# Kernel optimization log

Hardware: AMD Instinct MI355X
Metric: run time of the kernel (lower is better)

The kernel has to match this reference:

```python
import jax, jax.numpy as jnp
import numpy as np

EMBED_DIM = 768
NUM_HEADS = 12
HEAD_DIM = EMBED_DIM // NUM_HEADS
B, S = 2, 2048


def setup_inputs() -> dict:
    key = jax.random.key(0)
    k1, k2, k3, k4, k5 = jax.random.split(key, 5)
    scale = 1.0 / np.sqrt(EMBED_DIM)
    return {
        "x": jax.random.normal(k1, (B, S, EMBED_DIM), dtype=jnp.float32),
        "w_qkv": jax.random.normal(k2, (EMBED_DIM, 3 * EMBED_DIM), dtype=jnp.float32) * scale,
        "b_qkv": jax.random.normal(k3, (3 * EMBED_DIM,), dtype=jnp.float32) * 0.01,
        "w_proj": jax.random.normal(k4, (EMBED_DIM, EMBED_DIM), dtype=jnp.float32) * scale,
        "b_proj": jax.random.normal(k5, (EMBED_DIM,), dtype=jnp.float32) * 0.01,
    }


def reference(x, w_qkv, b_qkv, w_proj, b_proj):
    b, s, e = x.shape
    h, d = NUM_HEADS, HEAD_DIM
    # fused QKV projection: [b, s, 3, h, d]
    qkv = (x @ w_qkv + b_qkv).reshape(b, s, 3, h, d)
    q = qkv[:, :, 0].transpose(0, 2, 1, 3)  # [b, h, s, d]
    k = qkv[:, :, 1].transpose(0, 2, 1, 3)
    v = qkv[:, :, 2].transpose(0, 2, 1, 3)
    scores = jnp.einsum("bhqd,bhkd->bhqk", q, k) * (d ** -0.5)
    attn = jax.nn.softmax(scores, axis=-1)  # dropout is identity in eval mode
    out = jnp.einsum("bhqk,bhkd->bhqd", attn, v)
    out = out.transpose(0, 2, 1, 3).reshape(b, s, e)
    return out @ w_proj + b_proj
```

## Files before the change

### kernel.cpp

```cpp
#include <hip/hip_runtime.h>
#include <hip/hip_bf16.h>


typedef __bf16 bf16x8 __attribute__((ext_vector_type(8)));
typedef float f32x4 __attribute__((ext_vector_type(4)));
typedef unsigned short ushortx8 __attribute__((ext_vector_type(8)));
typedef unsigned short ushortx4 __attribute__((ext_vector_type(4)));
typedef unsigned int uintx4 __attribute__((ext_vector_type(4)));

#define EMB 768
#define SEQ 2048
#define NHEAD 12
#define HDIM 64
#define MROWS 4096
#define NQKV 2304
#define QSCALE 0.18033688011112042f

static __device__ __forceinline__ unsigned short b16(float f) {
  __hip_bfloat16 h = __float2bfloat16(f);
  return __builtin_bit_cast(unsigned short, h);
}

static __device__ __forceinline__ unsigned int cvtpk(float lo, float hi) {
  unsigned int r;
  asm("v_cvt_pk_bf16_f32 %0, %1, %2" : "=v"(r) : "v"(lo), "v"(hi));
  return r;
}

static __device__ __forceinline__ void gld16(const void* g, void* l) {
  __builtin_amdgcn_global_load_lds((const __attribute__((address_space(1))) void*)g,
                                   (__attribute__((address_space(3))) void*)l, 16, 0, 0);
}

__global__ __launch_bounds__(256) void k_prep(
    const float* __restrict__ x, const float* __restrict__ wqkv, const float* __restrict__ wproj,
    unsigned short* __restrict__ xb, unsigned short* __restrict__ wqkvT,
    unsigned short* __restrict__ wprojT) {
  __shared__ float t[64][65];
  const int bid = blockIdx.x;
  const int tid = threadIdx.x;
  if (bid < 1536) {
    int i = (bid * 256 + tid) * 8;
    f32x4 v0 = *(const f32x4*)(x + i);
    f32x4 v1 = *(const f32x4*)(x + i + 4);
    ushortx8 o;
    o[0] = b16(v0[0]); o[1] = b16(v0[1]); o[2] = b16(v0[2]); o[3] = b16(v0[3]);
    o[4] = b16(v1[0]); o[5] = b16(v1[1]); o[6] = b16(v1[2]); o[7] = b16(v1[3]);
    *(ushortx8*)(xb + i) = o;
    return;
  }
  const float* in; unsigned short* out; int N, bx, by;
  if (bid < 1536 + 432) { in = wqkv;  out = wqkvT;  N = NQKV; int r = bid - 1536; bx = r % 36; by = r / 36; }
  else                  { in = wproj; out = wprojT; N = EMB;  int r = bid - 1968; bx = r % 12; by = r / 12; }
  const int n0 = bx * 64, k0 = by * 64;
  const int xx = tid & 63, y0 = tid >> 6;
  #pragma unroll
  for (int i = 0; i < 16; ++i) { int r = y0 * 16 + i; t[r][xx] = in[(size_t)(k0 + r) * N + n0 + xx]; }
  __syncthreads();
  const int ks = tid & 7;
  const int nr0 = tid >> 3;
  #pragma unroll
  for (int i = 0; i < 2; ++i) {
    int nr = nr0 + i * 32;
    ushortx8 o;
    #pragma unroll
    for (int j = 0; j < 8; ++j) o[j] = b16(t[ks * 8 + j][nr]);
    *(ushortx8*)(out + (size_t)(n0 + nr) * EMB + k0 + ks * 8) = o;
  }
}

static __device__ __forceinline__ void gemm_tile_128(
    const unsigned short* __restrict__ A, const unsigned short* __restrict__ B,
    int K, int bm, int bn, char* lA, char* lB, f32x4 acc[4][4]) {
  const int tid = threadIdx.x, lane = tid & 63, w = tid >> 6;
  const int l15 = lane & 15, lg = lane >> 4;
  const int wm = w >> 1, wn = w & 1;
  #pragma unroll
  for (int m = 0; m < 4; ++m)
    #pragma unroll
    for (int n = 0; n < 4; ++n)
      acc[m][n] = (f32x4){0.f, 0.f, 0.f, 0.f};

  const int srow = w * 32 + (lane >> 3);
  const int glog = (lane & 7) ^ (lane >> 3);
  const size_t abase = (size_t)(bm * 128 + srow) * K + glog * 8;
  const size_t bbase = (size_t)(bn * 128 + srow) * K + glog * 8;
  const char* aB = lA + (wm * 64 + l15) * 128;
  const char* bB = lB + (wn * 64 + l15) * 128;
  const int rsw = (l15 & 7) << 4;

  const int T = K >> 6;
  {
    char* ad = lA + w * 4096; char* bd = lB + w * 4096;
    #pragma unroll
    for (int j = 0; j < 4; ++j) {
      gld16(A + abase + (size_t)j * 8 * K, ad + j * 1024);
      gld16(B + bbase + (size_t)j * 8 * K, bd + j * 1024);
    }
  }
  for (int t = 0; t < T; ++t) {
    const int cur = t & 1;
    if (t + 1 < T) {
      const int k1 = (t + 1) << 6;
      char* ad = lA + (cur ^ 1) * 16384 + w * 4096;
      char* bd = lB + (cur ^ 1) * 16384 + w * 4096;
      #pragma unroll
      for (int j = 0; j < 4; ++j) {
        gld16(A + abase + (size_t)j * 8 * K + k1, ad + j * 1024);
        gld16(B + bbase + (size_t)j * 8 * K + k1, bd + j * 1024);
      }
      asm volatile("s_waitcnt vmcnt(8)" ::: "memory");
    } else {
      asm volatile("s_waitcnt vmcnt(0)" ::: "memory");
    }
    __builtin_amdgcn_s_barrier();
    const char* ab = aB + cur * 16384;
    const char* bb = bB + cur * 16384;
    bf16x8 af[2][4], bfr[2][4];
    #pragma unroll
    for (int kk = 0; kk < 2; ++kk) {
      #pragma unroll
      for (int m = 0; m < 4; ++m)
        af[kk][m] = *(const bf16x8*)(ab + m * 2048 + (((kk * 4 + lg) * 16) ^ rsw));
      #pragma unroll
      for (int n = 0; n < 4; ++n)
        bfr[kk][n] = *(const bf16x8*)(bb + n * 2048 + (((kk * 4 + lg) * 16) ^ rsw));
    }
    #pragma unroll
    for (int kk = 0; kk < 2; ++kk)
      #pragma unroll
      for (int m = 0; m < 4; ++m)
        #pragma unroll
        for (int n = 0; n < 4; ++n)
          acc[m][n] = __builtin_amdgcn_mfma_f32_16x16x32_bf16(af[kk][m], bfr[kk][n], acc[m][n], 0, 0, 0);
    if (t + 1 < T) __builtin_amdgcn_s_barrier();
  }
}

static __device__ __forceinline__ int kvperm(int s) {
  return (s & ~0x1C) | ((s & 0x0C) << 1) | ((s & 0x10) >> 2);
}

__global__ __launch_bounds__(256) void k_gemm_qkv(
    const unsigned short* __restrict__ Xb, const unsigned short* __restrict__ Wt,
    const float* __restrict__ bias,
    unsigned short* __restrict__ Qb, unsigned short* __restrict__ Kb,
    unsigned short* __restrict__ VTb) {
  __shared__ __align__(16) char Alds[2 * 16384];
  __shared__ __align__(16) char Blds[2 * 16384];
  f32x4 acc[4][4];
  const int bm = blockIdx.x, bn = blockIdx.y;
  gemm_tile_128(Xb, Wt, EMB, bm, bn, Alds, Blds, acc);
  const int tid = threadIdx.x, lane = tid & 63, w = tid >> 6;
  const int l15 = lane & 15, lg = lane >> 4, wm = w >> 1, wn = w & 1;
  const int treg = bn / 6;
  if (treg < 2) {
    #pragma unroll
    for (int m = 0; m < 4; ++m)
      #pragma unroll
      for (int n = 0; n < 4; ++n)
        #pragma unroll
        for (int r = 0; r < 4; ++r) {
          int gr = bm * 128 + wm * 64 + m * 16 + lg * 4 + r;
          int gc = bn * 128 + wn * 64 + n * 16 + l15;
          float v = acc[m][n][r] + bias[gc];
          int rem = gc - treg * 768;
          int h = rem >> 6, d = rem & 63;
          int b = gr >> 11, s = gr & 2047;
          size_t off = ((size_t)(b * 12 + h) * 2048 + s) * 64 + d;
          if (treg == 0) Qb[off] = b16(v * QSCALE);
          else           Kb[off] = b16(v);
        }
  } else {
    #pragma unroll
    for (int m = 0; m < 4; ++m)
      #pragma unroll
      for (int n = 0; n < 4; ++n) {
        int gr0 = bm * 128 + wm * 64 + m * 16 + lg * 4;
        int gc = bn * 128 + wn * 64 + n * 16 + l15;
        int rem = gc - 1536;
        int h = rem >> 6, d = rem & 63;
        int b = gr0 >> 11, s0 = gr0 & 2047;
        int sp0 = kvperm(s0);
        ushortx4 o;
        #pragma unroll
        for (int r = 0; r < 4; ++r) o[r] = b16(acc[m][n][r] + bias[gc]);
        *(ushortx4*)(VTb + ((size_t)(b * 12 + h) * 64 + d) * 2048 + sp0) = o;
      }
  }
}

__global__ __launch_bounds__(256) void k_gemm_proj(
    const unsigned short* __restrict__ Ab, const unsigned short* __restrict__ Wt,
    const float* __restrict__ bias, float* __restrict__ out) {
  __shared__ __align__(16) char Alds[2 * 16384];
  __shared__ __align__(16) char Blds[2 * 16384];
  f32x4 acc[4][4];
  const int bm = blockIdx.x, bn = blockIdx.y;
  gemm_tile_128(Ab, Wt, EMB, bm, bn, Alds, Blds, acc);
  const int tid = threadIdx.x, lane = tid & 63, w = tid >> 6;
  const int l15 = lane & 15, lg = lane >> 4, wm = w >> 1, wn = w & 1;
  #pragma unroll
  for (int m = 0; m < 4; ++m)
    #pragma unroll
    for (int n = 0; n < 4; ++n)
      #pragma unroll
      for (int r = 0; r < 4; ++r) {
        int gr = bm * 128 + wm * 64 + m * 16 + lg * 4 + r;
        int gc = bn * 128 + wn * 64 + n * 16 + l15;
        out[(size_t)gr * EMB + gc] = acc[m][n][r] + bias[gc];
      }
}

__global__ __launch_bounds__(256) void k_attn(
    const unsigned short* __restrict__ Qg, const unsigned short* __restrict__ Kg,
    const unsigned short* __restrict__ VTg, unsigned short* __restrict__ AO) {
  __shared__ __align__(16) char KL[3 * 8192];
  __shared__ __align__(16) char VTL[3 * 8192];
  const int bid = blockIdx.x;
  const int slot = bid >> 3;
  const int bh = (bid & 7) * 3 + slot / 32;
  const int qt = slot & 31;
  const int b = bh / 12, h = bh % 12;
  const size_t base = (size_t)bh * (SEQ * HDIM);
  const int tid = threadIdx.x, lane = tid & 63, w = tid >> 6;
  const int l15 = lane & 15, lg = lane >> 4;
  const int swz = (l15 & 7) << 4;

  bf16x8 qf[2];
  {
    const size_t qoff = base + (size_t)(qt * 64 + w * 16 + l15) * 64 + lg * 8;
    qf[0] = *(const bf16x8*)(Qg + qoff);
    qf[1] = *(const bf16x8*)(Qg + qoff + 32);
  }

  const int srow0 = tid >> 3;
  const int scg0 = (tid & 7) ^ (srow0 & 7);
  const int scg1 = (tid & 7) ^ ((srow0 + 32) & 7);

  #define ASTAGE(tt, buf) do {                                                         \
    const int kv_ = (tt) * 64;                                                         \
    char* kd_ = KL + (buf) * 8192 + w * 1024;                                          \
    char* vd_ = VTL + (buf) * 8192 + w * 1024;                                         \
    gld16(Kg + base + (size_t)(kv_ + srow0) * 64 + scg0 * 8,           kd_);           \
    gld16(Kg + base + (size_t)(kv_ + srow0 + 32) * 64 + scg1 * 8,      kd_ + 4096);    \
    gld16(VTg + base + (size_t)srow0 * 2048 + kv_ + scg0 * 8,          vd_);           \
    gld16(VTg + base + (size_t)(srow0 + 32) * 2048 + kv_ + scg1 * 8,   vd_ + 4096);    \
  } while (0)

  f32x4 Oacc[4];
  #pragma unroll
  for (int nd = 0; nd < 4; ++nd) Oacc[nd] = (f32x4){0.f, 0.f, 0.f, 0.f};
  float l_ = 0.f;

  ASTAGE(0, 0);
  ASTAGE(1, 1);
  asm volatile("s_waitcnt vmcnt(4)" ::: "memory");
  __builtin_amdgcn_s_barrier();

  int cur = 0, pre = 2;
  for (int t = 0; t < 32; ++t) {
    if (t + 2 < 32) ASTAGE(t + 2, pre);
    const char* kb = KL + cur * 8192;
    const char* vb = VTL + cur * 8192;

    f32x4 sv[4];
    __builtin_amdgcn_s_setprio(1);
    #pragma unroll
    for (int n = 0; n < 4; ++n) {
      const char* rb = kb + (n * 16 + l15) * 128;
      bf16x8 kf0 = *(const bf16x8*)(rb + ((lg * 16) ^ swz));
      bf16x8 kf1 = *(const bf16x8*)(rb + ((64 + lg * 16) ^ swz));
      f32x4 z = (f32x4){0.f, 0.f, 0.f, 0.f};
      z = __builtin_amdgcn_mfma_f32_16x16x32_bf16(kf0, qf[0], z, 0, 0, 0);
      sv[n] = __builtin_amdgcn_mfma_f32_16x16x32_bf16(kf1, qf[1], z, 0, 0, 0);
    }

    #pragma unroll
    for (int c = 0; c < 2; ++c) {
      float pa0 = __builtin_amdgcn_exp2f(sv[2 * c][0]);
      float pa1 = __builtin_amdgcn_exp2f(sv[2 * c][1]);
      float pa2 = __builtin_amdgcn_exp2f(sv[2 * c][2]);
      float pa3 = __builtin_amdgcn_exp2f(sv[2 * c][3]);
      float pb0 = __builtin_amdgcn_exp2f(sv[2 * c + 1][0]);
      float pb1 = __builtin_amdgcn_exp2f(sv[2 * c + 1][1]);
      float pb2 = __builtin_amdgcn_exp2f(sv[2 * c + 1][2]);
      float pb3 = __builtin_amdgcn_exp2f(sv[2 * c + 1][3]);
      l_ += ((pa0 + pa1) + (pa2 + pa3)) + ((pb0 + pb1) + (pb2 + pb3));
      uintx4 uw;
      uw[0] = cvtpk(pa0, pa1);
      uw[1] = cvtpk(pa2, pa3);
      uw[2] = cvtpk(pb0, pb1);
      uw[3] = cvtpk(pb2, pb3);
      bf16x8 pfB = __builtin_bit_cast(bf16x8, uw);
      #pragma unroll
      for (int nd = 0; nd < 4; ++nd) {
        const char* vr = vb + (nd * 16 + l15) * 128;
        bf16x8 vf = *(const bf16x8*)(vr + ((c * 64 + lg * 16) ^ swz));
        Oacc[nd] = __builtin_amdgcn_mfma_f32_16x16x32_bf16(vf, pfB, Oacc[nd], 0, 0, 0);
      }
    }
    __builtin_amdgcn_s_setprio(0);

    if (t < 31) {
      if (t < 30) asm volatile("s_waitcnt vmcnt(4)" ::: "memory");
      else        asm volatile("s_waitcnt vmcnt(0)" ::: "memory");
      __builtin_amdgcn_s_barrier();
    }
    cur = (cur == 2) ? 0 : cur + 1;
    pre = (pre == 2) ? 0 : pre + 1;
  }
  #undef ASTAGE

  l_ += __shfl_xor(l_, 16);
  l_ += __shfl_xor(l_, 32);
  const float rl = 1.0f / l_;
  const int q = qt * 64 + w * 16 + l15;
  #pragma unroll
  for (int nd = 0; nd < 4; ++nd) {
    ushortx4 o;
    #pragma unroll
    for (int r = 0; r < 4; ++r) o[r] = b16(Oacc[nd][r] * rl);
    *(ushortx4*)(AO + ((size_t)(b * 2048 + q)) * EMB + h * 64 + nd * 16 + lg * 4) = o;
  }
}

extern "C" void kernel_launch(void* const* d_in, const int* in_sizes, int n_in,
                              void* d_out, int out_size, void* d_ws, size_t ws_size,
                              hipStream_t stream) {
  const float* x     = (const float*)d_in[0];
  const float* wqkv  = (const float*)d_in[1];
  const float* bqkv  = (const float*)d_in[2];
  const float* wproj = (const float*)d_in[3];
  const float* bproj = (const float*)d_in[4];
  float* out = (float*)d_out;
  char* ws = (char*)d_ws;

  unsigned short* xb     = (unsigned short*)(ws + 0);
  unsigned short* wqkvT  = (unsigned short*)(ws + 6291456);
  unsigned short* wprojT = (unsigned short*)(ws + 9830400);
  unsigned short* Qb     = (unsigned short*)(ws + 11010048);
  unsigned short* Kb     = (unsigned short*)(ws + 17301504);
  unsigned short* VTb    = (unsigned short*)(ws + 23592960);
  unsigned short* AOb    = (unsigned short*)(ws + 29884416);

  k_prep<<<2112, 256, 0, stream>>>(x, wqkv, wproj, xb, wqkvT, wprojT);
  k_gemm_qkv<<<dim3(MROWS / 128, NQKV / 128), 256, 0, stream>>>(xb, wqkvT, bqkv, Qb, Kb, VTb);
  k_attn<<<24 * (SEQ / 64), 256, 0, stream>>>(Qb, Kb, VTb, AOb);
  k_gemm_proj<<<dim3(MROWS / 128, EMB / 128), 256, 0, stream>>>(AOb, wprojT, bproj, out);
}
```

Before: 89.77 us.

## Load V fragments directly from global into registers instead of LDS staging

The attention kernel drops the LDS triple-buffer for the transposed V tile. Each wave now loads its V MFMA fragments straight from global memory at the start of every KV iteration, so the loads overlap the QK MFMAs and the softmax. The wait counts and barrier placement are adjusted because each async stage now issues two loads instead of four. This halves LDS use and removes the LDS reads for V, but every wave fetches the same V tile again, and the global load latency is hidden only by one iteration's compute rather than by the two-stage prefetch.

New measurement: 150.6 us. 67.8% more time.

```diff
diff --git a/kernel.cpp b/kernel.cpp
--- a/kernel.cpp
+++ b/kernel.cpp
@@ -216,7 +216,6 @@
     const unsigned short* __restrict__ Qg, const unsigned short* __restrict__ Kg,
     const unsigned short* __restrict__ VTg, unsigned short* __restrict__ AO) {
   __shared__ __align__(16) char KL[3 * 8192];
-  __shared__ __align__(16) char VTL[3 * 8192];
   const int bid = blockIdx.x;
   const int slot = bid >> 3;
   const int bh = (bid & 7) * 3 + slot / 32;
@@ -241,12 +240,14 @@
   #define ASTAGE(tt, buf) do {                                                         \
     const int kv_ = (tt) * 64;                                                         \
     char* kd_ = KL + (buf) * 8192 + w * 1024;                                          \
-    char* vd_ = VTL + (buf) * 8192 + w * 1024;                                         \
     gld16(Kg + base + (size_t)(kv_ + srow0) * 64 + scg0 * 8,           kd_);           \
     gld16(Kg + base + (size_t)(kv_ + srow0 + 32) * 64 + scg1 * 8,      kd_ + 4096);    \
-    gld16(VTg + base + (size_t)srow0 * 2048 + kv_ + scg0 * 8,          vd_);           \
-    gld16(VTg + base + (size_t)(srow0 + 32) * 2048 + kv_ + scg1 * 8,   vd_ + 4096);    \
   } while (0)
+
+  const unsigned short* vrow[4];
+  #pragma unroll
+  for (int nd = 0; nd < 4; ++nd)
+    vrow[nd] = VTg + base + (size_t)(nd * 16 + l15) * 2048 + lg * 8;
 
   f32x4 Oacc[4];
   #pragma unroll
@@ -255,15 +256,21 @@
 
   ASTAGE(0, 0);
   ASTAGE(1, 1);
-  asm volatile("s_waitcnt vmcnt(4)" ::: "memory");
+  asm volatile("s_waitcnt vmcnt(2)" ::: "memory");
   __builtin_amdgcn_s_barrier();
 
   int cur = 0, pre = 2;
   for (int t = 0; t < 32; ++t) {
+    const int kv0 = t * 64;
+    bf16x8 vf[8];
+    #pragma unroll
+    for (int c = 0; c < 2; ++c)
+      #pragma unroll
+      for (int nd = 0; nd < 4; ++nd)
+        vf[c * 4 + nd] = *(const bf16x8*)(vrow[nd] + kv0 + c * 32);
     if (t + 2 < 32) ASTAGE(t + 2, pre);
+
     const char* kb = KL + cur * 8192;
-    const char* vb = VTL + cur * 8192;
-
     f32x4 sv[4];
     __builtin_amdgcn_s_setprio(1);
     #pragma unroll
@@ -276,6 +283,7 @@
       sv[n] = __builtin_amdgcn_mfma_f32_16x16x32_bf16(kf1, qf[1], z, 0, 0, 0);
     }
 
+    bf16x8 pf[2];
     #pragma unroll
     for (int c = 0; c < 2; ++c) {
       float pa0 = __builtin_amdgcn_exp2f(sv[2 * c][0]);
@@ -292,21 +300,19 @@
       uw[1] = cvtpk(pa2, pa3);
       uw[2] = cvtpk(pb0, pb1);
       uw[3] = cvtpk(pb2, pb3);
-      bf16x8 pfB = __builtin_bit_cast(bf16x8, uw);
-      #pragma unroll
-      for (int nd = 0; nd < 4; ++nd) {
-        const char* vr = vb + (nd * 16 + l15) * 128;
-        bf16x8 vf = *(const bf16x8*)(vr + ((c * 64 + lg * 16) ^ swz));
-        Oacc[nd] = __builtin_amdgcn_mfma_f32_16x16x32_bf16(vf, pfB, Oacc[nd], 0, 0, 0);
-      }
-    }
+      pf[c] = __builtin_bit_cast(bf16x8, uw);
+    }
+
+    if (t < 30) asm volatile("s_waitcnt vmcnt(2)" ::: "memory");
+    else        asm volatile("s_waitcnt vmcnt(0)" ::: "memory");
+    #pragma unroll
+    for (int c = 0; c < 2; ++c)
+      #pragma unroll
+      for (int nd = 0; nd < 4; ++nd)
+        Oacc[nd] = __builtin_amdgcn_mfma_f32_16x16x32_bf16(vf[c * 4 + nd], pf[c], Oacc[nd], 0, 0, 0);
     __builtin_amdgcn_s_setprio(0);
 
-    if (t < 31) {
-      if (t < 30) asm volatile("s_waitcnt vmcnt(4)" ::: "memory");
-      else        asm volatile("s_waitcnt vmcnt(0)" ::: "memory");
-      __builtin_amdgcn_s_barrier();
-    }
+    if (t < 31) __builtin_amdgcn_s_barrier();
     cur = (cur == 2) ? 0 : cur + 1;
     pre = (pre == 2) ? 0 : pre + 1;
   }
```
